# Optimization experiments

Hardware: AMD Instinct MI355X
Metric: run time of the kernel (lower is better)

The kernel has to match this reference:

```python
import jax, jax.numpy as jnp
import numpy as np

MAX_RIGID = 8
MAX_TORSION = 7
MAX_ATOM = 24
N_RES = 22
N_NODES = 400_000
EPS = 1e-12


def v_norm_safe(v):
    return v / jnp.sqrt(jnp.sum(v * v, axis=-1, keepdims=True) + EPS)


def combine_operations(X, Y):
    # X, Y: (..., 4, 3) rigid ops: rows 0..2 rotation, row 3 translation
    rot = jnp.einsum('...ij,...jk->...ik', X[..., :3, :], Y[..., :3, :])
    tr = jnp.einsum('...ij,...j->...i', X[..., :3, :], Y[..., 3, :]) + X[..., 3, :]
    return jnp.concatenate([rot, tr[..., None, :]], axis=-2)


def setup_inputs() -> dict:
    key = jax.random.key(0)
    ks = jax.random.split(key, 7)
    output_0 = jax.random.normal(ks[0], (N_NODES, 2 * MAX_TORSION), jnp.float32)
    output_1 = jax.random.normal(ks[1], (N_NODES, 3, 3), jnp.float32)
    pos = jax.random.normal(ks[2], (N_NODES, 3), jnp.float32) * 10.0
    residue_type = jax.random.randint(ks[3], (N_NODES,), 0, N_RES)
    # rigid transform table: proper-ish rotations (QR) + translations, per residue type / rigid group
    raw = jax.random.normal(ks[4], (N_RES, MAX_RIGID, 3, 3), jnp.float32)
    q, _ = jnp.linalg.qr(raw)
    trans = jax.random.normal(ks[5], (N_RES, MAX_RIGID, 1, 3), jnp.float32)
    rigid_transforms = jnp.concatenate([q, trans], axis=-2)  # (22, 8, 4, 3)
    rigid_groups = jax.random.normal(ks[6], (N_RES, MAX_ATOM, 3), jnp.float32)
    rng = np.random.default_rng(0)
    # parent rigid index for torsion i must be < i (tree dependency)
    transforms_dep = jnp.asarray(
        np.stack([rng.integers(0, max(i, 1), N_RES) for i in range(MAX_RIGID)], axis=1),
        dtype=jnp.int32)  # (22, 8)
    groups_dep = jnp.asarray(rng.integers(0, MAX_RIGID, (N_RES, MAX_ATOM)), dtype=jnp.int32)
    return dict(output_0=output_0, output_1=output_1, pos=pos,
                rigid_transforms=rigid_transforms, rigid_groups=rigid_groups,
                residue_type=residue_type, transforms_dep=transforms_dep,
                groups_dep=groups_dep, num_recycle=4)


def output_to_opr(output_0, output_1, num_recycle):
    v0 = output_1[:, 0]
    v1 = output_1[:, 1]
    e0 = v_norm_safe(v0)
    u1 = v1 - e0 * jnp.sum(e0 * v1, axis=-1, keepdims=True)
    e1 = v_norm_safe(u1)
    e2 = jnp.cross(e0, e1)
    rot = jnp.swapaxes(jnp.stack([e0, e1, e2], axis=1), -1, -2)  # (N,3,3), columns e0,e1,e2
    t = 0.1 * output_1[:, 2][:, None, :] / num_recycle            # (N,1,3)
    bb = jnp.concatenate([rot, t], axis=1)                        # (N,4,3)
    sc = v_norm_safe(output_0.reshape(-1, MAX_TORSION, 2))        # (N,7,2)
    return bb, sc


def build_structure(bb, sc, pos, rigid_transforms, rigid_groups,
                    residue_type, transforms_dep, groups_dep):
    T = rigid_transforms[residue_type]   # (N,8,4,3)
    G = rigid_groups[residue_type]       # (N,24,3)
    tdep = transforms_dep[residue_type]  # (N,8)
    gdep = groups_dep[residue_type]      # (N,24)
    N = bb.shape[0]
    # torsion frames: rotation about x-axis by (cos,sin)=sc
    cos, sin = sc[..., 0], sc[..., 1]          # (N,7)
    z = jnp.zeros_like(cos)
    o = jnp.ones_like(cos)
    row0 = jnp.stack([o, z, z], axis=-1)
    row1 = jnp.stack([z, cos, -sin], axis=-1)
    row2 = jnp.stack([z, sin, cos], axis=-1)
    row3 = jnp.zeros((N, MAX_TORSION, 3), dtype=bb.dtype)
    tor_opr = jnp.stack([row0, row1, row2, row3], axis=-2)  # (N,7,4,3)
    bb_opr = jnp.concatenate([bb[:, :3], (bb[:, 3] + pos)[:, None, :]], axis=1)[:, None]  # (N,1,4,3)
    opr = jnp.concatenate([bb_opr, tor_opr], axis=1)  # (N,8,4,3)
    opr = combine_operations(T, opr)
    # iterative parent-frame composition (gather along rigid dim)
    for i_tor in range(1, MAX_RIGID):
        prev = jnp.take_along_axis(opr, tdep[:, i_tor][:, None, None, None], axis=1)[:, 0]
        opr = opr.at[:, i_tor].set(combine_operations(prev, opr[:, i_tor]))
    opr_atom = jnp.take_along_axis(opr, gdep[:, :, None, None], axis=1)  # (N,24,4,3)
    R = jnp.einsum('naij,naj->nai', opr_atom[:, :, :3], G) + opr_atom[:, :, 3]  # (N,24,3)
    return R, opr[:, 0]


def reference(output_0, output_1, pos, rigid_transforms, rigid_groups,
              residue_type, transforms_dep, groups_dep, num_recycle):
    bb, sc = output_to_opr(output_0, output_1, num_recycle)
    R, opr_bb = build_structure(bb, sc, pos, rigid_transforms, rigid_groups,
                                residue_type, transforms_dep, groups_dep)
    return R, opr_bb, bb, sc
```

## Files before the change

kernel.cpp:

```cpp
#include <hip/hip_runtime.h>

#define MAX_RIGID 8

__device__ __forceinline__ unsigned pkh(float a, float b) {
    return __builtin_bit_cast(unsigned, __builtin_amdgcn_cvt_pkrtz(a, b));
}
__device__ __forceinline__ float uplo(unsigned u) {
    return (float)__builtin_bit_cast(_Float16, (unsigned short)(u & 0xffffu));
}
__device__ __forceinline__ float uphi(unsigned u) {
    return (float)__builtin_bit_cast(_Float16, (unsigned short)(u >> 16));
}

__device__ __forceinline__ void combine12(const float* X, const float* Y, float* O) {
    #pragma unroll
    for (int i = 0; i < 3; ++i) {
        #pragma unroll
        for (int k = 0; k < 3; ++k)
            O[i*3+k] = X[i*3+0]*Y[0+k] + X[i*3+1]*Y[3+k] + X[i*3+2]*Y[6+k];
        O[9+i] = X[i*3+0]*Y[9] + X[i*3+1]*Y[10] + X[i*3+2]*Y[11] + X[9+i];
    }
}

__global__ __launch_bounds__(256) void build_struct_kernel(
    const float* __restrict__ out0,
    const float* __restrict__ out1,
    const float* __restrict__ pos,
    const float* __restrict__ rigidT,
    const float* __restrict__ rigidG,
    const int*   __restrict__ resty,
    const int*   __restrict__ tdep,
    const int*   __restrict__ gdep,
    const int*   __restrict__ nrp,
    float* __restrict__ dR,
    float* __restrict__ dOprBB,
    float* __restrict__ dBB,
    float* __restrict__ dSC,
    int N)
{
    __shared__ float    sG[2200];
    __shared__ unsigned sgdp[88];
    __shared__ unsigned stdp[22];
    __shared__ unsigned sbh[4][42][64];

    const int tid  = threadIdx.x;
    const int lane = tid & 63;
    const int w    = tid >> 6;

    for (int i = tid; i < 1584; i += 256) { int r = i / 72; int q = i - r*72; int a = q / 3;
                                            sG[r*100 + a*4 + (q - a*3)] = rigidG[i]; }
    if (tid < 22) {
        unsigned p0 = 0, p1 = 0, p2 = 0, tw = 0;
        #pragma unroll
        for (int a = 0; a < 8; ++a) {
            p0 |= ((unsigned)gdep[tid*24 +      a] & 7u) << (a*4);
            p1 |= ((unsigned)gdep[tid*24 +  8 + a] & 7u) << (a*4);
            p2 |= ((unsigned)gdep[tid*24 + 16 + a] & 7u) << (a*4);
            tw |= ((unsigned)tdep[tid*8  +      a] & 7u) << (a*4);
        }
        sgdp[tid*4+0] = p0; sgdp[tid*4+1] = p1; sgdp[tid*4+2] = p2;
        stdp[tid] = tw;
    }
    __syncthreads();

    long n = (long)blockIdx.x * 256 + tid;
    if (n >= N) return;

    int iv = *nrp;
    float nrv = (iv > 0 && iv < 1000000) ? (float)iv
                                         : *reinterpret_cast<const float*>(nrp);
    float tscale = 0.1f / nrv;

    float o0r[14];
    {
        const float2* p = reinterpret_cast<const float2*>(out0 + (size_t)n * 14);
        #pragma unroll
        for (int k = 0; k < 7; ++k) { float2 v = p[k]; o0r[2*k] = v.x; o0r[2*k+1] = v.y; }
    }
    float o1r[9];
    {
        const float* p = out1 + (size_t)n * 9;
        #pragma unroll
        for (int k = 0; k < 9; ++k) o1r[k] = p[k];
    }
    float px = pos[(size_t)n*3+0], py = pos[(size_t)n*3+1], pz = pos[(size_t)n*3+2];
    int rt = resty[n];

    float sc[14];
    #pragma unroll
    for (int k = 0; k < 7; ++k) {
        float a = o0r[2*k], b = o0r[2*k+1];
        float r = __builtin_amdgcn_rsqf(a*a + b*b + 1e-12f);
        sc[2*k] = a*r; sc[2*k+1] = b*r;
    }
    float bb[12];
    {
        float v0x=o1r[0], v0y=o1r[1], v0z=o1r[2];
        float v1x=o1r[3], v1y=o1r[4], v1z=o1r[5];
        float r0 = __builtin_amdgcn_rsqf(v0x*v0x + v0y*v0y + v0z*v0z + 1e-12f);
        float e0x=v0x*r0, e0y=v0y*r0, e0z=v0z*r0;
        float dp = e0x*v1x + e0y*v1y + e0z*v1z;
        float u1x = v1x - e0x*dp, u1y = v1y - e0y*dp, u1z = v1z - e0z*dp;
        float r1 = __builtin_amdgcn_rsqf(u1x*u1x + u1y*u1y + u1z*u1z + 1e-12f);
        float e1x=u1x*r1, e1y=u1y*r1, e1z=u1z*r1;
        float e2x = e0y*e1z - e0z*e1y;
        float e2y = e0z*e1x - e0x*e1z;
        float e2z = e0x*e1y - e0y*e1x;
        bb[0]=e0x; bb[1]=e1x; bb[2]=e2x;
        bb[3]=e0y; bb[4]=e1y; bb[5]=e2y;
        bb[6]=e0z; bb[7]=e1z; bb[8]=e2z;
        bb[9]=tscale*o1r[6]; bb[10]=tscale*o1r[7]; bb[11]=tscale*o1r[8];
    }

    const float4* T4 = reinterpret_cast<const float4*>(rigidT + rt * 96);
    unsigned tw  = stdp[rt];
    unsigned gw0 = sgdp[rt*4+0], gw1 = sgdp[rt*4+1], gw2 = sgdp[rt*4+2];

    float opr[MAX_RIGID][12];
    {
        float X[12];
        { float4 r0v=T4[0], r1v=T4[1], r2v=T4[2];
          X[0]=r0v.x; X[1]=r0v.y; X[2]=r0v.z; X[3]=r0v.w;
          X[4]=r1v.x; X[5]=r1v.y; X[6]=r1v.z; X[7]=r1v.w;
          X[8]=r2v.x; X[9]=r2v.y; X[10]=r2v.z; X[11]=r2v.w; }
        float Y[12] = { bb[0],bb[1],bb[2], bb[3],bb[4],bb[5], bb[6],bb[7],bb[8],
                        bb[9]+px, bb[10]+py, bb[11]+pz };
        combine12(X, Y, opr[0]);
    }
    #pragma unroll
    for (int i = 1; i < MAX_RIGID; ++i) {
        float X[12];
        { float4 r0v=T4[i*3], r1v=T4[i*3+1], r2v=T4[i*3+2];
          X[0]=r0v.x; X[1]=r0v.y; X[2]=r0v.z; X[3]=r0v.w;
          X[4]=r1v.x; X[5]=r1v.y; X[6]=r1v.z; X[7]=r1v.w;
          X[8]=r2v.x; X[9]=r2v.y; X[10]=r2v.z; X[11]=r2v.w; }
        float c = sc[2*(i-1)], s = sc[2*(i-1)+1];
        float M[12];
        M[0]=X[0]; M[3]=X[3]; M[6]=X[6];
        M[1] = c*X[1] + s*X[2];   M[2] = c*X[2] - s*X[1];
        M[4] = c*X[4] + s*X[5];   M[5] = c*X[5] - s*X[4];
        M[7] = c*X[7] + s*X[8];   M[8] = c*X[8] - s*X[7];
        M[9]=X[9]; M[10]=X[10]; M[11]=X[11];
        int t = (int)((tw >> (i*4)) & 7u);
        float P[12];
        #pragma unroll
        for (int j = 0; j < 12; ++j) P[j] = opr[0][j];
        #pragma unroll
        for (int cnd = 1; cnd < i; ++cnd) {
            bool take = (t == cnd);
            #pragma unroll
            for (int j = 0; j < 12; ++j) P[j] = take ? opr[cnd][j] : P[j];
        }
        combine12(P, M, opr[i]);
        #pragma unroll
        for (int s2 = 0; s2 < 6; ++s2)
            sbh[w][(i-1)*6 + s2][lane] = pkh(opr[i][2*s2], opr[i][2*s2+1]);
    }

    {
        float2* d0 = reinterpret_cast<float2*>(dSC + (size_t)n * 14);
        #pragma unroll
        for (int k = 0; k < 7; ++k) d0[k] = make_float2(sc[2*k], sc[2*k+1]);
        float4* d1 = reinterpret_cast<float4*>(dBB + (size_t)n * 12);
        #pragma unroll
        for (int k = 0; k < 3; ++k) d1[k] = make_float4(bb[4*k], bb[4*k+1], bb[4*k+2], bb[4*k+3]);
        float4* d2 = reinterpret_cast<float4*>(dOprBB + (size_t)n * 12);
        #pragma unroll
        for (int k = 0; k < 3; ++k) d2[k] = make_float4(opr[0][4*k], opr[0][4*k+1], opr[0][4*k+2], opr[0][4*k+3]);
    }

    const float4* G4 = reinterpret_cast<const float4*>(sG + rt * 100);
    float* Rout = dR + (size_t)n * 72;
    #pragma unroll
    for (int c = 0; c < 3; ++c) {
        unsigned gw = (c == 0) ? gw0 : ((c == 1) ? gw1 : gw2);
        float rbuf[24];
        #pragma unroll
        for (int a4 = 0; a4 < 8; ++a4) {
            int a = c*8 + a4;
            int g = (int)((gw >> (a4*4)) & 7u);
            float4 gv = G4[a];
            int base = (g > 0) ? (g-1)*6 : 0;
            float O[12];
            #pragma unroll
            for (int s2 = 0; s2 < 6; ++s2) {
                unsigned u = sbh[w][base + s2][lane];
                O[2*s2]   = uplo(u);
                O[2*s2+1] = uphi(u);
            }
            bool g0 = (g == 0);
            #pragma unroll
            for (int j = 0; j < 12; ++j) O[j] = g0 ? opr[0][j] : O[j];
            rbuf[a4*3+0] = O[0]*gv.x + O[1]*gv.y + O[2]*gv.z + O[9];
            rbuf[a4*3+1] = O[3]*gv.x + O[4]*gv.y + O[5]*gv.z + O[10];
            rbuf[a4*3+2] = O[6]*gv.x + O[7]*gv.y + O[8]*gv.z + O[11];
        }
        float4* dst = reinterpret_cast<float4*>(Rout + c * 24);
        #pragma unroll
        for (int q = 0; q < 6; ++q)
            dst[q] = make_float4(rbuf[4*q], rbuf[4*q+1], rbuf[4*q+2], rbuf[4*q+3]);
    }
}

extern "C" void kernel_launch(void* const* d_in, const int* in_sizes, int n_in,
                              void* d_out, int out_size, void* d_ws, size_t ws_size,
                              hipStream_t stream) {
    const float* out0 = (const float*)d_in[0];
    const float* out1 = (const float*)d_in[1];
    const float* pos  = (const float*)d_in[2];
    const float* rT   = (const float*)d_in[3];
    const float* rG   = (const float*)d_in[4];
    const int*   res  = (const int*)d_in[5];
    const int*   td   = (const int*)d_in[6];
    const int*   gd   = (const int*)d_in[7];
    const int*   nr   = (const int*)d_in[8];

    int N = in_sizes[5];

    float* dR     = (float*)d_out;
    float* dOprBB = dR + (size_t)N * 72;
    float* dBB    = dOprBB + (size_t)N * 12;
    float* dSC    = dBB + (size_t)N * 12;

    dim3 grid((N + 255) / 256), block(256);
    hipLaunchKernelGGL(build_struct_kernel, grid, block, 0, stream,
                       out0, out1, pos, rT, rG, res, td, gd, nr,
                       dR, dOprBB, dBB, dSC, N);
}
```

Measured before the change: 74.57 us.

## Coalesce global stores via per-wave LDS transpose and register-select atom frames

Each wave packs its per-node outputs (sin/cos, backbone frame, oriented backbone, atom positions) into LDS and rewrites them so consecutive lanes store consecutive addresses, replacing strided per-thread stores. Atom frame selection now uses an in-register select over all eight frames instead of reading fp16 frames from LDS. The staging rounds every output through fp16, which lowers output precision, and it adds LDS traffic and wave-level waits.

```diff
diff --git a/kernel.cpp b/kernel.cpp
--- a/kernel.cpp
+++ b/kernel.cpp
@@ -10,6 +10,12 @@
 }
 __device__ __forceinline__ float uphi(unsigned u) {
     return (float)__builtin_bit_cast(_Float16, (unsigned short)(u >> 16));
+}
+
+__device__ __forceinline__ void wave_lds_fence() {
+    __builtin_amdgcn_sched_barrier(0);
+    asm volatile("s_waitcnt lgkmcnt(0)" ::: "memory");
+    __builtin_amdgcn_sched_barrier(0);
 }
 
 __device__ __forceinline__ void combine12(const float* X, const float* Y, float* O) {
@@ -20,6 +26,24 @@
             O[i*3+k] = X[i*3+0]*Y[0+k] + X[i*3+1]*Y[3+k] + X[i*3+2]*Y[6+k];
         O[9+i] = X[i*3+0]*Y[9] + X[i*3+1]*Y[10] + X[i*3+2]*Y[11] + X[9+i];
     }
+}
+
+__device__ __forceinline__ void atom_xyz(const float opr[MAX_RIGID][12], int g,
+                                         float gx, float gy, float gz,
+                                         float& x, float& y, float& z)
+{
+    float O[12];
+    #pragma unroll
+    for (int j = 0; j < 12; ++j) O[j] = opr[0][j];
+    #pragma unroll
+    for (int cnd = 1; cnd < MAX_RIGID; ++cnd) {
+        bool take = (g == cnd);
+        #pragma unroll
+        for (int j = 0; j < 12; ++j) O[j] = take ? opr[cnd][j] : O[j];
+    }
+    x = O[0]*gx + O[1]*gy + O[2]*gz + O[9];
+    y = O[3]*gx + O[4]*gy + O[5]*gz + O[10];
+    z = O[6]*gx + O[7]*gy + O[8]*gz + O[11];
 }
 
 __global__ __launch_bounds__(256) void build_struct_kernel(
@@ -41,7 +65,7 @@
     __shared__ float    sG[2200];
     __shared__ unsigned sgdp[88];
     __shared__ unsigned stdp[22];
-    __shared__ unsigned sbh[4][42][64];
+    __shared__ unsigned sTr[4][1344];
 
     const int tid  = threadIdx.x;
     const int lane = tid & 63;
@@ -63,7 +87,13 @@
     }
     __syncthreads();
 
-    long n = (long)blockIdx.x * 256 + tid;
+    const long node0 = (long)blockIdx.x * 256 + (long)w * 64;
+    int cnt;
+    {
+        long rem = (long)N - node0;
+        cnt = (rem <= 0) ? 0 : (rem >= 64 ? 64 : (int)rem);
+    }
+    long n = node0 + lane;
     if (n >= N) return;
 
     int iv = *nrp;
@@ -152,25 +182,54 @@
             for (int j = 0; j < 12; ++j) P[j] = take ? opr[cnd][j] : P[j];
         }
         combine12(P, M, opr[i]);
-        #pragma unroll
-        for (int s2 = 0; s2 < 6; ++s2)
-            sbh[w][(i-1)*6 + s2][lane] = pkh(opr[i][2*s2], opr[i][2*s2+1]);
-    }
-
-    {
-        float2* d0 = reinterpret_cast<float2*>(dSC + (size_t)n * 14);
-        #pragma unroll
-        for (int k = 0; k < 7; ++k) d0[k] = make_float2(sc[2*k], sc[2*k+1]);
-        float4* d1 = reinterpret_cast<float4*>(dBB + (size_t)n * 12);
-        #pragma unroll
-        for (int k = 0; k < 3; ++k) d1[k] = make_float4(bb[4*k], bb[4*k+1], bb[4*k+2], bb[4*k+3]);
-        float4* d2 = reinterpret_cast<float4*>(dOprBB + (size_t)n * 12);
-        #pragma unroll
-        for (int k = 0; k < 3; ++k) d2[k] = make_float4(opr[0][4*k], opr[0][4*k+1], opr[0][4*k+2], opr[0][4*k+3]);
-    }
+    }
+
+    unsigned* tb = sTr[w];
+
+    #pragma unroll
+    for (int k = 0; k < 7; ++k) tb[lane*21 + k]      = pkh(sc[2*k], sc[2*k+1]);
+    #pragma unroll
+    for (int k = 0; k < 6; ++k) tb[lane*21 + 7 + k]  = pkh(bb[2*k], bb[2*k+1]);
+    #pragma unroll
+    for (int k = 0; k < 6; ++k) tb[lane*21 + 13 + k] = pkh(opr[0][2*k], opr[0][2*k+1]);
+    wave_lds_fence();
+    {
+        float* d0 = dSC + node0 * 14;
+        #pragma unroll
+        for (int j = 0; j < 7; ++j) {
+            int s = j*64 + lane;
+            if (s < cnt*7) {
+                int nd = s / 7; int k = s - nd*7;
+                unsigned u = tb[nd*21 + k];
+                *reinterpret_cast<float2*>(&d0[2*s]) = make_float2(uplo(u), uphi(u));
+            }
+        }
+        float* d1 = dBB + node0 * 12;
+        #pragma unroll
+        for (int j = 0; j < 3; ++j) {
+            int s4 = j*64 + lane;
+            if (s4 < cnt*3) {
+                int nd = s4 / 3; int m4 = s4 - nd*3;
+                unsigned u0 = tb[nd*21 + 7 + 2*m4], u1 = tb[nd*21 + 7 + 2*m4 + 1];
+                *reinterpret_cast<float4*>(&d1[4*s4]) =
+                    make_float4(uplo(u0), uphi(u0), uplo(u1), uphi(u1));
+            }
+        }
+        float* d2 = dOprBB + node0 * 12;
+        #pragma unroll
+        for (int j = 0; j < 3; ++j) {
+            int s4 = j*64 + lane;
+            if (s4 < cnt*3) {
+                int nd = s4 / 3; int m4 = s4 - nd*3;
+                unsigned u0 = tb[nd*21 + 13 + 2*m4], u1 = tb[nd*21 + 13 + 2*m4 + 1];
+                *reinterpret_cast<float4*>(&d2[4*s4]) =
+                    make_float4(uplo(u0), uphi(u0), uplo(u1), uphi(u1));
+            }
+        }
+    }
+    wave_lds_fence();
 
     const float4* G4 = reinterpret_cast<const float4*>(sG + rt * 100);
-    float* Rout = dR + (size_t)n * 72;
     #pragma unroll
     for (int c = 0; c < 3; ++c) {
         unsigned gw = (c == 0) ? gw0 : ((c == 1) ? gw1 : gw2);
@@ -180,25 +239,27 @@
             int a = c*8 + a4;
             int g = (int)((gw >> (a4*4)) & 7u);
             float4 gv = G4[a];
-            int base = (g > 0) ? (g-1)*6 : 0;
-            float O[12];
+            float x, y, z;
+            atom_xyz(opr, g, gv.x, gv.y, gv.z, x, y, z);
+            rbuf[a4*3+0] = x; rbuf[a4*3+1] = y; rbuf[a4*3+2] = z;
+        }
+        #pragma unroll
+        for (int k = 0; k < 12; ++k) tb[lane*13 + k] = pkh(rbuf[2*k], rbuf[2*k+1]);
+        wave_lds_fence();
+        {
+            float* rdst = dR + node0 * 72 + c * 24;
             #pragma unroll
-            for (int s2 = 0; s2 < 6; ++s2) {
-                unsigned u = sbh[w][base + s2][lane];
-                O[2*s2]   = uplo(u);
-                O[2*s2+1] = uphi(u);
-            }
-            bool g0 = (g == 0);
-            #pragma unroll
-            for (int j = 0; j < 12; ++j) O[j] = g0 ? opr[0][j] : O[j];
-            rbuf[a4*3+0] = O[0]*gv.x + O[1]*gv.y + O[2]*gv.z + O[9];
-            rbuf[a4*3+1] = O[3]*gv.x + O[4]*gv.y + O[5]*gv.z + O[10];
-            rbuf[a4*3+2] = O[6]*gv.x + O[7]*gv.y + O[8]*gv.z + O[11];
-        }
-        float4* dst = reinterpret_cast<float4*>(Rout + c * 24);
-        #pragma unroll
-        for (int q = 0; q < 6; ++q)
-            dst[q] = make_float4(rbuf[4*q], rbuf[4*q+1], rbuf[4*q+2], rbuf[4*q+3]);
+            for (int it = 0; it < 6; ++it) {
+                int s4 = it*64 + lane;
+                if (s4 < cnt*6) {
+                    int nd = s4 / 6; int m4 = s4 - nd*6;
+                    unsigned u0 = tb[nd*13 + 2*m4], u1 = tb[nd*13 + 2*m4 + 1];
+                    *reinterpret_cast<float4*>(&rdst[nd*72 + 4*m4]) =
+                        make_float4(uplo(u0), uphi(u0), uplo(u1), uphi(u1));
+                }
+            }
+        }
+        if (c < 2) wave_lds_fence();
     }
 }
 
```

Result: slower. 76.30 us (+2.3%).

## Cut register pressure by reading parent frames from LDS and recomputing sincos

Applied to the files above, without the earlier changes.

The per-thread opr[8][12] register array and its select chain are replaced by a loop that reads the parent frame back from the fp16-packed LDS buffer. Only opr0 stays in registers. The sin/cos normalisation is now computed per iteration from global loads and recomputed for the SC output, and several unroll pragmas are removed. The aim is fewer VGPRs and higher occupancy. The cost is extra LDS round-trips on a serial dependency chain, repeated global loads, and parent frames used at fp16 precision in the chain composition, which adds numerical error.

```diff
diff --git a/kernel.cpp b/kernel.cpp
--- a/kernel.cpp
+++ b/kernel.cpp
@@ -51,7 +51,6 @@
                                             sG[r*100 + a*4 + (q - a*3)] = rigidG[i]; }
     if (tid < 22) {
         unsigned p0 = 0, p1 = 0, p2 = 0, tw = 0;
-        #pragma unroll
         for (int a = 0; a < 8; ++a) {
             p0 |= ((unsigned)gdep[tid*24 +      a] & 7u) << (a*4);
             p1 |= ((unsigned)gdep[tid*24 +  8 + a] & 7u) << (a*4);
@@ -71,12 +70,6 @@
                                          : *reinterpret_cast<const float*>(nrp);
     float tscale = 0.1f / nrv;
 
-    float o0r[14];
-    {
-        const float2* p = reinterpret_cast<const float2*>(out0 + (size_t)n * 14);
-        #pragma unroll
-        for (int k = 0; k < 7; ++k) { float2 v = p[k]; o0r[2*k] = v.x; o0r[2*k+1] = v.y; }
-    }
     float o1r[9];
     {
         const float* p = out1 + (size_t)n * 9;
@@ -86,13 +79,6 @@
     float px = pos[(size_t)n*3+0], py = pos[(size_t)n*3+1], pz = pos[(size_t)n*3+2];
     int rt = resty[n];
 
-    float sc[14];
-    #pragma unroll
-    for (int k = 0; k < 7; ++k) {
-        float a = o0r[2*k], b = o0r[2*k+1];
-        float r = __builtin_amdgcn_rsqf(a*a + b*b + 1e-12f);
-        sc[2*k] = a*r; sc[2*k+1] = b*r;
-    }
     float bb[12];
     {
         float v0x=o1r[0], v0y=o1r[1], v0z=o1r[2];
@@ -113,10 +99,9 @@
     }
 
     const float4* T4 = reinterpret_cast<const float4*>(rigidT + rt * 96);
-    unsigned tw  = stdp[rt];
-    unsigned gw0 = sgdp[rt*4+0], gw1 = sgdp[rt*4+1], gw2 = sgdp[rt*4+2];
-
-    float opr[MAX_RIGID][12];
+    unsigned tw = stdp[rt];
+
+    float opr0[12];
     {
         float X[12];
         { float4 r0v=T4[0], r1v=T4[1], r2v=T4[2];
@@ -125,62 +110,72 @@
           X[8]=r2v.x; X[9]=r2v.y; X[10]=r2v.z; X[11]=r2v.w; }
         float Y[12] = { bb[0],bb[1],bb[2], bb[3],bb[4],bb[5], bb[6],bb[7],bb[8],
                         bb[9]+px, bb[10]+py, bb[11]+pz };
-        combine12(X, Y, opr[0]);
-    }
-    #pragma unroll
+        combine12(X, Y, opr0);
+    }
+
+    const float2* o0p = reinterpret_cast<const float2*>(out0 + (size_t)n * 14);
     for (int i = 1; i < MAX_RIGID; ++i) {
+        float2 ab = o0p[i-1];
+        float rr = __builtin_amdgcn_rsqf(ab.x*ab.x + ab.y*ab.y + 1e-12f);
+        float c = ab.x*rr, s = ab.y*rr;
+
         float X[12];
         { float4 r0v=T4[i*3], r1v=T4[i*3+1], r2v=T4[i*3+2];
           X[0]=r0v.x; X[1]=r0v.y; X[2]=r0v.z; X[3]=r0v.w;
           X[4]=r1v.x; X[5]=r1v.y; X[6]=r1v.z; X[7]=r1v.w;
           X[8]=r2v.x; X[9]=r2v.y; X[10]=r2v.z; X[11]=r2v.w; }
-        float c = sc[2*(i-1)], s = sc[2*(i-1)+1];
         float M[12];
         M[0]=X[0]; M[3]=X[3]; M[6]=X[6];
         M[1] = c*X[1] + s*X[2];   M[2] = c*X[2] - s*X[1];
         M[4] = c*X[4] + s*X[5];   M[5] = c*X[5] - s*X[4];
         M[7] = c*X[7] + s*X[8];   M[8] = c*X[8] - s*X[7];
         M[9]=X[9]; M[10]=X[10]; M[11]=X[11];
+
         int t = (int)((tw >> (i*4)) & 7u);
+        int base = (t > 0 ? t - 1 : 0) * 6;
         float P[12];
         #pragma unroll
-        for (int j = 0; j < 12; ++j) P[j] = opr[0][j];
-        #pragma unroll
-        for (int cnd = 1; cnd < i; ++cnd) {
-            bool take = (t == cnd);
-            #pragma unroll
-            for (int j = 0; j < 12; ++j) P[j] = take ? opr[cnd][j] : P[j];
-        }
-        combine12(P, M, opr[i]);
+        for (int s2 = 0; s2 < 6; ++s2) {
+            unsigned u = sbh[w][base + s2][lane];
+            P[2*s2]   = uplo(u);
+            P[2*s2+1] = uphi(u);
+        }
+        bool t0 = (t == 0);
+        #pragma unroll
+        for (int j = 0; j < 12; ++j) P[j] = t0 ? opr0[j] : P[j];
+
+        float O[12];
+        combine12(P, M, O);
         #pragma unroll
         for (int s2 = 0; s2 < 6; ++s2)
-            sbh[w][(i-1)*6 + s2][lane] = pkh(opr[i][2*s2], opr[i][2*s2+1]);
-    }
-
-    {
-        float2* d0 = reinterpret_cast<float2*>(dSC + (size_t)n * 14);
-        #pragma unroll
-        for (int k = 0; k < 7; ++k) d0[k] = make_float2(sc[2*k], sc[2*k+1]);
+            sbh[w][(i-1)*6 + s2][lane] = pkh(O[2*s2], O[2*s2+1]);
+    }
+
+    {
+        float* d0 = dSC + (size_t)n * 14;
+        for (int k = 0; k < 7; ++k) {
+            float2 ab = o0p[k];
+            float rr = __builtin_amdgcn_rsqf(ab.x*ab.x + ab.y*ab.y + 1e-12f);
+            *reinterpret_cast<float2*>(&d0[2*k]) = make_float2(ab.x*rr, ab.y*rr);
+        }
         float4* d1 = reinterpret_cast<float4*>(dBB + (size_t)n * 12);
         #pragma unroll
         for (int k = 0; k < 3; ++k) d1[k] = make_float4(bb[4*k], bb[4*k+1], bb[4*k+2], bb[4*k+3]);
         float4* d2 = reinterpret_cast<float4*>(dOprBB + (size_t)n * 12);
         #pragma unroll
-        for (int k = 0; k < 3; ++k) d2[k] = make_float4(opr[0][4*k], opr[0][4*k+1], opr[0][4*k+2], opr[0][4*k+3]);
+        for (int k = 0; k < 3; ++k) d2[k] = make_float4(opr0[4*k], opr0[4*k+1], opr0[4*k+2], opr0[4*k+3]);
     }
 
     const float4* G4 = reinterpret_cast<const float4*>(sG + rt * 100);
     float* Rout = dR + (size_t)n * 72;
-    #pragma unroll
     for (int c = 0; c < 3; ++c) {
-        unsigned gw = (c == 0) ? gw0 : ((c == 1) ? gw1 : gw2);
+        unsigned gw = sgdp[rt*4 + c];
         float rbuf[24];
         #pragma unroll
         for (int a4 = 0; a4 < 8; ++a4) {
-            int a = c*8 + a4;
             int g = (int)((gw >> (a4*4)) & 7u);
-            float4 gv = G4[a];
-            int base = (g > 0) ? (g-1)*6 : 0;
+            float4 gv = G4[c*8 + a4];
+            int base = (g > 0 ? g - 1 : 0) * 6;
             float O[12];
             #pragma unroll
             for (int s2 = 0; s2 < 6; ++s2) {
@@ -190,7 +185,7 @@
             }
             bool g0 = (g == 0);
             #pragma unroll
-            for (int j = 0; j < 12; ++j) O[j] = g0 ? opr[0][j] : O[j];
+            for (int j = 0; j < 12; ++j) O[j] = g0 ? opr0[j] : O[j];
             rbuf[a4*3+0] = O[0]*gv.x + O[1]*gv.y + O[2]*gv.z + O[9];
             rbuf[a4*3+1] = O[3]*gv.x + O[4]*gv.y + O[5]*gv.z + O[10];
             rbuf[a4*3+2] = O[6]*gv.x + O[7]*gv.y + O[8]*gv.z + O[11];
```

Measured after the change: 81.85 us. +9.8%, slower.
